# Kernel tuning notes

Hardware: AMD Instinct MI355X
Metric: run time of the kernel (lower is better)

The kernel has to match this reference:

```python
import jax, jax.numpy as jnp
import numpy as np

N = 65536      # total nodes (cells) in batch
E = 262144     # edges per edge type
T = 3          # edge types: row, col, diag
D = 128        # hidden_dim
HG = 4         # gat_heads
DHG = D // HG  # 32, GAT head dim
HH = 4         # hgt_heads
DHH = D // HH  # 32, HGT head dim
B = 32         # boards per batch
SLOPE = 0.2
EPS = 1e-6


def setup_inputs():
    ks = jax.random.split(jax.random.key(0), 32)
    def nrm(i, shape, s=0.05):
        return (jax.random.normal(ks[i], shape) * s).astype(jnp.float32)
    inp = {
        'x_cell': nrm(0, (N, D), 1.0),
        'z_h': nrm(1, (B, D), 1.0),
        'x_cell_embedded': nrm(2, (N, D), 1.0),
        'edge_index': jax.random.randint(ks[3], (T, 2, E), 0, N, dtype=jnp.int32),
        'batch_size': B,
        # GAT conv 1 (one GATConv per edge type, summed)
        'gat1_W': nrm(4, (T, D, D), 0.09),
        'gat1_asrc': nrm(5, (T, HG, DHG), 0.12),
        'gat1_adst': nrm(6, (T, HG, DHG), 0.12),
        'gat1_b': jnp.zeros((T, D), jnp.float32),
        # GAT conv 2
        'gat2_W': nrm(7, (T, D, D), 0.09),
        'gat2_asrc': nrm(8, (T, HG, DHG), 0.12),
        'gat2_adst': nrm(9, (T, HG, DHG), 0.12),
        'gat2_b': jnp.zeros((T, D), jnp.float32),
        # RMSNorms
        'norm1_s': jnp.ones((D,), jnp.float32),
        'norm2_s': jnp.ones((D,), jnp.float32),
        'norm3_s': jnp.ones((D,), jnp.float32),
        # HGT (single node type 'cell', T edge types)
        'hgt_Wk': nrm(10, (D, D), 0.09), 'hgt_bk': jnp.zeros((D,), jnp.float32),
        'hgt_Wq': nrm(11, (D, D), 0.09), 'hgt_bq': jnp.zeros((D,), jnp.float32),
        'hgt_Wv': nrm(12, (D, D), 0.09), 'hgt_bv': jnp.zeros((D,), jnp.float32),
        'hgt_arel': nrm(13, (T, HH, DHH, DHH), 0.15),
        'hgt_mrel': nrm(14, (T, HH, DHH, DHH), 0.15),
        'hgt_prel': jnp.ones((T, HH), jnp.float32),
        'hgt_Wo': nrm(15, (D, D), 0.09), 'hgt_bo': jnp.zeros((D,), jnp.float32),
        'hgt_skip': jnp.ones((), jnp.float32),
        # input injection
        'inj_W': nrm(16, (D, D), 0.09), 'inj_b': jnp.zeros((D,), jnp.float32),
        # FiLM
        'film_W1': nrm(17, (D, 2 * D), 0.09), 'film_b1': jnp.zeros((2 * D,), jnp.float32),
        'film_W2': nrm(18, (2 * D, 2 * D), 0.001), 'film_b2': jnp.zeros((2 * D,), jnp.float32),
    }
    return inp


def _rmsnorm(x, scale):
    return scale * x * jax.lax.rsqrt(jnp.mean(x * x, axis=-1, keepdims=True) + EPS)


def _res(x_old, x_new, scale):
    return jax.nn.leaky_relu(x_old + _rmsnorm(x_new, scale), SLOPE)


def _gat_sum(x, W, asrc, adst, b, src, dst):
    """HeteroConv(sum) over T GATConvs (concat heads, add_self_loops)."""
    loop = jnp.arange(N, dtype=src.dtype)
    def one(Wt, a_s, a_d, bt, s, t):
        s = jnp.concatenate([s, loop])   # self loops
        t = jnp.concatenate([t, loop])
        h = (x @ Wt).reshape(N, HG, DHG)             # [N,H,Dh]
        alpha_src = (h * a_s).sum(-1)                # [N,H]
        alpha_dst = (h * a_d).sum(-1)
        e = jax.nn.leaky_relu(alpha_src[s] + alpha_dst[t], SLOPE)  # [E+N,H]
        m = jax.ops.segment_max(e, t, num_segments=N)
        ex = jnp.exp(e - m[t])
        denom = jax.ops.segment_sum(ex, t, num_segments=N)
        alpha = ex / (denom[t] + 1e-16)
        out = jax.ops.segment_sum(alpha[:, :, None] * h[s], t, num_segments=N)
        return out.reshape(N, D) + bt
    return jax.vmap(one)(W, asrc, adst, b, src, dst).sum(0)


def _hgt(x, Wk, bk, Wq, bq, Wv, bv, a_rel, m_rel, p_rel, Wo, bo, skip, src, dst):
    k = (x @ Wk + bk).reshape(N, HH, DHH)
    q = (x @ Wq + bq).reshape(N, HH, DHH)
    v = (x @ Wv + bv).reshape(N, HH, DHH)
    # per-edge-type relation transforms at node level, then gather per edge
    k_t = jnp.einsum('nhd,thdf->tnhf', k, a_rel)    # [T,N,H,Dk]
    v_t = jnp.einsum('nhd,thdf->tnhf', v, m_rel)
    k_e = jax.vmap(lambda a, i: a[i])(k_t, src)     # [T,E,H,Dk]
    v_e = jax.vmap(lambda a, i: a[i])(v_t, src)
    score = (q[dst] * k_e).sum(-1) * p_rel[:, None, :] / np.sqrt(DHH)  # [T,E,H]
    score = score.reshape(T * E, HH)
    dst_f = dst.reshape(-1)
    m = jax.ops.segment_max(score, dst_f, num_segments=N)
    ex = jnp.exp(score - m[dst_f])
    denom = jax.ops.segment_sum(ex, dst_f, num_segments=N)
    alpha = ex / (denom[dst_f] + 1e-16)
    agg = jax.ops.segment_sum(alpha[:, :, None] * v_e.reshape(T * E, HH, DHH),
                              dst_f, num_segments=N)          # [N,H,Dk]
    out = jax.nn.gelu(agg.reshape(N, D), approximate=False) @ Wo + bo
    sig = jax.nn.sigmoid(skip)
    return sig * out + (1.0 - sig) * x


def _film(nodes, z_h, W1, b1, W2, b2, bsz):
    gb = jax.nn.gelu(z_h @ W1 + b1, approximate=False) @ W2 + b2  # [B,2D]
    gamma, beta = jnp.split(gb, 2, axis=-1)
    gamma = 0.1 * jnp.tanh(gamma)
    beta = 0.1 * jnp.tanh(beta)
    c = N // bsz
    out = (1.0 + gamma)[:, None, :] * nodes.reshape(bsz, c, D) + beta[:, None, :]
    return out.reshape(N, D)


def reference(x_cell, z_h, x_cell_embedded,
              gat1_W, gat1_asrc, gat1_adst, gat1_b,
              gat2_W, gat2_asrc, gat2_adst, gat2_b,
              norm1_s, norm2_s, norm3_s,
              hgt_Wk, hgt_bk, hgt_Wq, hgt_bq, hgt_Wv, hgt_bv,
              hgt_arel, hgt_mrel, hgt_prel, hgt_Wo, hgt_bo, hgt_skip,
              inj_W, inj_b, film_W1, film_b1, film_W2, film_b2,
              edge_index, batch_size):
    src = edge_index[:, 0]
    dst = edge_index[:, 1]
    x1 = _res(x_cell, _gat_sum(x_cell, gat1_W, gat1_asrc, gat1_adst, gat1_b, src, dst), norm1_s)
    x2 = _res(x1, _gat_sum(x1, gat2_W, gat2_asrc, gat2_adst, gat2_b, src, dst), norm2_s)
    x3 = _res(x2, _hgt(x2, hgt_Wk, hgt_bk, hgt_Wq, hgt_bq, hgt_Wv, hgt_bv,
                       hgt_arel, hgt_mrel, hgt_prel, hgt_Wo, hgt_bo, hgt_skip,
                       src, dst), norm3_s)
    x3 = x3 + x_cell_embedded @ inj_W + inj_b
    return _film(x3, z_h, film_W1, film_b1, film_W2, film_b2, batch_size)
```

## Files before the change

### kernel.cpp

```cpp
#include <hip/hip_runtime.h>

#define NN 65536
#define EE 262144
#define ND ((size_t)NN * 128)
#define TBW 132
#define WLP 136

typedef unsigned short u16;
typedef short bf8_t __attribute__((ext_vector_type(8)));
typedef float f32x4 __attribute__((ext_vector_type(4)));

__device__ __forceinline__ float lrelu(float x){ return x > 0.f ? x : 0.2f*x; }
__device__ __forceinline__ float gelu_exact(float x){ return 0.5f*x*(1.f+erff(x*0.70710678118654752f)); }
__device__ __forceinline__ u16 f2bf(float f){
    union { float f; unsigned u; } v; v.f = f;
    unsigned u = v.u;
    return (u16)((u + 0x7FFFu + ((u >> 16) & 1u)) >> 16);
}
__device__ __forceinline__ float bf2f(u16 b){
    union { unsigned u; float f; } v; v.u = ((unsigned)b) << 16; return v.f;
}
__device__ __forceinline__ float2 bf2x(unsigned p){
    union { unsigned u; float f; } a, b;
    a.u = (p & 0xFFFFu) << 16; b.u = p & 0xFFFF0000u;
    return make_float2(a.f, b.f);
}
__device__ __forceinline__ unsigned cvt2(float a, float b){
    unsigned r; asm("v_cvt_pk_bf16_f32 %0, %1, %2" : "=v"(r) : "v"(a), "v"(b)); return r;
}

__device__ __forceinline__ void load_af32(const float* __restrict__ X, int row, int lk, bf8_t* af){
    #pragma unroll
    for (int kk = 0; kk < 4; ++kk){
        const float* p = X + (size_t)row*128 + kk*32 + lk*8;
        float4 a = *(const float4*)p;
        float4 b = *(const float4*)(p+4);
        union { bf8_t v; unsigned u[4]; } r;
        r.u[0] = cvt2(a.x, a.y); r.u[1] = cvt2(a.z, a.w);
        r.u[2] = cvt2(b.x, b.y); r.u[3] = cvt2(b.z, b.w);
        af[kk] = r.v;
    }
}
__device__ __forceinline__ void load_af16(const u16* __restrict__ X, int row, int lk, bf8_t* af){
    #pragma unroll
    for (int kk = 0; kk < 4; ++kk)
        af[kk] = *(const bf8_t*)(X + (size_t)row*128 + kk*32 + lk*8);
}

__device__ __forceinline__ void stage_w(const u16* __restrict__ src, u16* __restrict__ wl, int tid){
    #pragma unroll
    for (int j = 0; j < 8; ++j){
        int o = (j*256 + tid)*8;
        bf8_t v = *(const bf8_t*)(src + o);
        *(bf8_t*)(wl + ((o>>7)*WLP + (o&127))) = v;
    }
}

__device__ __forceinline__ void mfma_l1_acc(const bf8_t* af, const u16* __restrict__ wl,
                                            int lr, int lk, f32x4* acc){
    #pragma unroll
    for (int kk = 0; kk < 4; ++kk){
        bf8_t B[8];
        #pragma unroll
        for (int nt = 0; nt < 8; ++nt)
            B[nt] = *(const bf8_t*)&wl[(nt*16+lr)*WLP + kk*32 + lk*8];
        #pragma unroll
        for (int nt = 0; nt < 8; ++nt)
            acc[nt] = __builtin_amdgcn_mfma_f32_16x16x32_bf16(af[kk], B[nt], acc[nt], 0, 0, 0);
    }
}
__device__ __forceinline__ void mfma_l2_acc(const bf8_t* af0, const bf8_t* af1,
                                            const u16* __restrict__ wl,
                                            int lr, int lk, f32x4* acc0, f32x4* acc1){
    #pragma unroll
    for (int kk = 0; kk < 4; ++kk){
        bf8_t B[8];
        #pragma unroll
        for (int nt = 0; nt < 8; ++nt)
            B[nt] = *(const bf8_t*)&wl[(nt*16+lr)*WLP + kk*32 + lk*8];
        #pragma unroll
        for (int nt = 0; nt < 8; ++nt){
            acc0[nt] = __builtin_amdgcn_mfma_f32_16x16x32_bf16(af0[kk], B[nt], acc0[nt], 0, 0, 0);
            acc1[nt] = __builtin_amdgcn_mfma_f32_16x16x32_bf16(af1[kk], B[nt], acc1[nt], 0, 0, 0);
        }
    }
}
__device__ __forceinline__ void mfma_l2(const bf8_t* af0, const bf8_t* af1,
                                        const u16* __restrict__ wl,
                                        int lr, int lk, f32x4* acc0, f32x4* acc1){
    #pragma unroll
    for (int i = 0; i < 8; ++i){ acc0[i] = (f32x4){0.f,0.f,0.f,0.f}; acc1[i] = (f32x4){0.f,0.f,0.f,0.f}; }
    mfma_l2_acc(af0, af1, wl, lr, lk, acc0, acc1);
}

__device__ __forceinline__ void acc_to_tb(u16 (*tbw)[TBW], const f32x4* acc, int lr, int lk, const float* bias){
    asm volatile("s_waitcnt lgkmcnt(0)" ::: "memory");
    #pragma unroll
    for (int nt = 0; nt < 8; ++nt){
        int col = nt*16 + lr;
        float badd = bias ? bias[col] : 0.f;
        #pragma unroll
        for (int i = 0; i < 4; ++i) tbw[lk*4+i][col] = f2bf(acc[nt][i] + badd);
    }
    asm volatile("s_waitcnt lgkmcnt(0)" ::: "memory");
}
__device__ __forceinline__ void acc_to_tb_gelu(u16 (*tbw)[TBW], const f32x4* acc, int lr, int lk){
    asm volatile("s_waitcnt lgkmcnt(0)" ::: "memory");
    #pragma unroll
    for (int nt = 0; nt < 8; ++nt){
        int col = nt*16 + lr;
        #pragma unroll
        for (int i = 0; i < 4; ++i) tbw[lk*4+i][col] = f2bf(gelu_exact(acc[nt][i]));
    }
    asm volatile("s_waitcnt lgkmcnt(0)" ::: "memory");
}
__device__ __forceinline__ void tb_store(const u16 (*tbw)[TBW], u16* __restrict__ O, size_t rowstride, int rowbase, int lr, int lk){
    #pragma unroll
    for (int c = 0; c < 4; ++c){
        bf8_t v = *(const bf8_t*)&tbw[c*4+lk][lr*8];
        *(bf8_t*)(O + (size_t)(rowbase + c*4 + lk)*rowstride + lr*8) = v;
    }
}
__device__ __forceinline__ void tb_frags(const u16 (*tbw)[TBW], int lr, int lk, bf8_t* ha){
    #pragma unroll
    for (int kk = 0; kk < 4; ++kk) ha[kk] = *(const bf8_t*)&tbw[lr][kk*32 + lk*8];
}
__device__ __forceinline__ void tb_rows(const u16 (*tbw)[TBW], int lr, int lk, bf8_t* rw){
    #pragma unroll
    for (int c = 0; c < 4; ++c) rw[c] = *(const bf8_t*)&tbw[c*4+lk][lr*8];
}

__global__ __launch_bounds__(256) void wpack_k(
    const float* __restrict__ g1W, const float* __restrict__ g2W,
    const float* __restrict__ Wk, const float* __restrict__ Wq, const float* __restrict__ Wv,
    const float* __restrict__ Wo, const float* __restrict__ injW,
    const float* __restrict__ arel, const float* __restrict__ mrel,
    const float* __restrict__ g1as, const float* __restrict__ g1ad,
    const float* __restrict__ g2as, const float* __restrict__ g2ad,
    u16* __restrict__ wp, u16* __restrict__ wpa)
{
    int b = blockIdx.x, tid = threadIdx.x;
    if (b < 17) {
        const float* src; int rel = 0;
        if (b < 3) src = g1W + b*16384;
        else if (b < 6) src = g2W + (b-3)*16384;
        else if (b == 6) src = Wk;
        else if (b == 7) src = Wq;
        else if (b == 8) src = Wv;
        else if (b == 9) src = Wo;
        else if (b == 10) src = injW;
        else if (b < 14) { src = arel + (b-11)*4096; rel = 2; }
        else { src = mrel + (b-14)*4096; rel = 1; }
        u16* dst = wp + (size_t)b*16384;
        for (int idx = tid; idx < 16384; idx += 256) {
            int n = idx >> 7, k = idx & 127;
            float v;
            if (rel == 1)      v = ((n>>5)==(k>>5)) ? src[(n>>5)*1024 + (k&31)*32 + (n&31)] : 0.f;
            else if (rel == 2) v = ((n>>5)==(k>>5)) ? src[(n>>5)*1024 + (n&31)*32 + (k&31)] : 0.f;
            else               v = src[k*128 + n];
            dst[idx] = f2bf(v);
        }
    } else {
        for (int idx = tid; idx < 6*2048; idx += 256) {
            int m = idx >> 11;
            int j = idx & 2047;
            int cg = j >> 7, k = j & 127;
            const float* as = (m < 3) ? g1as : g2as;
            const float* ad = (m < 3) ? g1ad : g2ad;
            int t = (m < 3) ? m : m - 3;
            float v = 0.f;
            if (cg < 4)      { if ((k>>5)==cg)   v = as[t*128 + cg*32 + (k&31)]; }
            else if (cg < 8) { int g = cg-4; if ((k>>5)==g) v = ad[t*128 + g*32 + (k&31)]; }
            wpa[idx] = f2bf(v);
        }
    }
}

template<int AF32>
__global__ __launch_bounds__(256, 2) void gat_gemm3_k(const float* __restrict__ Xf, const u16* __restrict__ Xb,
    const u16* __restrict__ wpg, const u16* __restrict__ wpa,
    u16* __restrict__ hb, float* __restrict__ alsb, float* __restrict__ aldb)
{
    __shared__ __align__(16) u16 wl[128*WLP];
    __shared__ __align__(16) u16 tb[4][16][TBW];
    const int tid = threadIdx.x, wave = tid>>6, lane = tid&63, lr = lane&15, lk = lane>>4;
    const int rw0 = blockIdx.x*128 + wave*32;
    bf8_t af0[4], af1[4];
    if (AF32){ load_af32(Xf, rw0 + lr, lk, af0); load_af32(Xf, rw0 + 16 + lr, lk, af1); }
    else     { load_af16(Xb, rw0 + lr, lk, af0); load_af16(Xb, rw0 + 16 + lr, lk, af1); }
    f32x4 acc0[8], acc1[8];
    for (int t = 0; t < 3; ++t) {
        __syncthreads();
        stage_w(wpg + t*16384, wl, tid);
        __syncthreads();
        mfma_l2(af0, af1, wl, lr, lk, acc0, acc1);
        bf8_t Ba[4];
        #pragma unroll
        for (int kk = 0; kk < 4; ++kk)
            Ba[kk] = *(const bf8_t*)&wpa[t*2048 + lr*128 + kk*32 + lk*8];
        u16* h = hb + (size_t)t*ND;
        float* alst = alsb + (size_t)t*NN*4;
        float* aldt = aldb + (size_t)t*NN*4;
        {
            acc_to_tb(tb[wave], acc0, lr, lk, nullptr);
            tb_store(tb[wave], h, 128, rw0, lr, lk);
            bf8_t ha[4]; tb_frags(tb[wave], lr, lk, ha);
            f32x4 a2 = (f32x4){0.f,0.f,0.f,0.f};
            #pragma unroll
            for (int kk = 0; kk < 4; ++kk)
                a2 = __builtin_amdgcn_mfma_f32_16x16x32_bf16(ha[kk], Ba[kk], a2, 0, 0, 0);
            if (lr < 8){
                float* dp = (lr < 4) ? alst : aldt;
                int g = lr & 3;
                #pragma unroll
                for (int i = 0; i < 4; ++i) dp[(size_t)(rw0 + lk*4 + i)*4 + g] = a2[i];
            }
        }
        {
            acc_to_tb(tb[wave], acc1, lr, lk, nullptr);
            tb_store(tb[wave], h, 128, rw0 + 16, lr, lk);
            bf8_t ha[4]; tb_frags(tb[wave], lr, lk, ha);
            f32x4 a2 = (f32x4){0.f,0.f,0.f,0.f};
            #pragma unroll
            for (int kk = 0; kk < 4; ++kk)
                a2 = __builtin_amdgcn_mfma_f32_16x16x32_bf16(ha[kk], Ba[kk], a2, 0, 0, 0);
            if (lr < 8){
                float* dp = (lr < 4) ? alst : aldt;
                int g = lr & 3;
                #pragma unroll
                for (int i = 0; i < 4; ++i) dp[(size_t)(rw0 + 16 + lk*4 + i)*4 + g] = a2[i];
            }
        }
    }
}

__global__ __launch_bounds__(256, 2) void hgt_proj_k(const u16* __restrict__ X,
    const u16* __restrict__ wpk, const u16* __restrict__ wpq, const u16* __restrict__ wpv,
    const u16* __restrict__ wparel,
    const float* __restrict__ bk, const float* __restrict__ bq, const float* __restrict__ bv,
    u16* __restrict__ kvb, u16* __restrict__ qtb)
{
    __shared__ __align__(16) u16 wl[128*WLP];
    __shared__ __align__(16) u16 tb[4][16][TBW];
    const int tid = threadIdx.x, wave = tid>>6, lane = tid&63, lr = lane&15, lk = lane>>4;
    const int rw0 = blockIdx.x*128 + wave*32;
    bf8_t af0[4], af1[4];
    load_af16(X, rw0 + lr, lk, af0);
    load_af16(X, rw0 + 16 + lr, lk, af1);
    f32x4 acc0[8], acc1[8];
    stage_w(wpk, wl, tid);
    __syncthreads();
    mfma_l2(af0, af1, wl, lr, lk, acc0, acc1);
    acc_to_tb(tb[wave], acc0, lr, lk, bk); tb_store(tb[wave], kvb, 256, rw0, lr, lk);
    acc_to_tb(tb[wave], acc1, lr, lk, bk); tb_store(tb[wave], kvb, 256, rw0 + 16, lr, lk);
    __syncthreads();
    stage_w(wpv, wl, tid);
    __syncthreads();
    mfma_l2(af0, af1, wl, lr, lk, acc0, acc1);
    acc_to_tb(tb[wave], acc0, lr, lk, bv); tb_store(tb[wave], kvb + 128, 256, rw0, lr, lk);
    acc_to_tb(tb[wave], acc1, lr, lk, bv); tb_store(tb[wave], kvb + 128, 256, rw0 + 16, lr, lk);
    __syncthreads();
    stage_w(wpq, wl, tid);
    __syncthreads();
    bf8_t ha0[4], ha1[4];
    mfma_l2(af0, af1, wl, lr, lk, acc0, acc1);
    acc_to_tb(tb[wave], acc0, lr, lk, bq); tb_frags(tb[wave], lr, lk, ha0);
    acc_to_tb(tb[wave], acc1, lr, lk, bq); tb_frags(tb[wave], lr, lk, ha1);
    for (int t = 0; t < 3; ++t){
        __syncthreads();
        stage_w(wparel + t*16384, wl, tid);
        __syncthreads();
        mfma_l2(ha0, ha1, wl, lr, lk, acc0, acc1);
        u16* o = qtb + (size_t)t*ND;
        acc_to_tb(tb[wave], acc0, lr, lk, nullptr); tb_store(tb[wave], o, 128, rw0, lr, lk);
        acc_to_tb(tb[wave], acc1, lr, lk, nullptr); tb_store(tb[wave], o, 128, rw0 + 16, lr, lk);
    }
}

__global__ __launch_bounds__(256) void hgt_agg_k(const u16* __restrict__ kvb,
    const u16* __restrict__ qtb, const float* __restrict__ prel,
    const int* __restrict__ coff, const int* __restrict__ csrc,
    u16* __restrict__ pb)
{
    int gid = blockIdx.x*256 + threadIdx.x;
    int node = gid >> 6, lane = gid & 63;
    int hh = lane >> 4;
    float a0[3], a1[3];
    float dsum = 0.f;
    #pragma unroll
    for (int t = 0; t < 3; ++t) {
        a0[t] = 0.f; a1[t] = 0.f;
        float ph = prel[t*4 + hh] * 0.17677669529663689f;
        float2 qv = bf2x(*(const unsigned*)&qtb[(size_t)t*ND + (size_t)node*128 + lane*2]);
        const int* cs = csrc + (size_t)t*EE;
        int beg = coff[t*(NN+1) + node], end = coff[t*(NN+1) + node + 1];
        int e = beg;
        for (; e + 4 <= end; e += 4) {
            int sA = cs[e], sB = cs[e+1], sC = cs[e+2], sD = cs[e+3];
            size_t rA = (size_t)sA*256 + lane*2, rB = (size_t)sB*256 + lane*2;
            size_t rC = (size_t)sC*256 + lane*2, rD = (size_t)sD*256 + lane*2;
            unsigned kA = *(const unsigned*)&kvb[rA], kB = *(const unsigned*)&kvb[rB];
            unsigned kC = *(const unsigned*)&kvb[rC], kD = *(const unsigned*)&kvb[rD];
            unsigned vA = *(const unsigned*)&kvb[rA+128], vB = *(const unsigned*)&kvb[rB+128];
            unsigned vC = *(const unsigned*)&kvb[rC+128], vD = *(const unsigned*)&kvb[rD+128];
            float2 k2A = bf2x(kA), k2B = bf2x(kB), k2C = bf2x(kC), k2D = bf2x(kD);
            float scA = qv.x*k2A.x + qv.y*k2A.y;
            float scB = qv.x*k2B.x + qv.y*k2B.y;
            float scC = qv.x*k2C.x + qv.y*k2C.y;
            float scD = qv.x*k2D.x + qv.y*k2D.y;
            #pragma unroll
            for (int o = 1; o < 16; o <<= 1){
                scA += __shfl_xor(scA, o); scB += __shfl_xor(scB, o);
                scC += __shfl_xor(scC, o); scD += __shfl_xor(scD, o);
            }
            float eA = expf(scA*ph), eB = expf(scB*ph), eC = expf(scC*ph), eD = expf(scD*ph);
            float2 v2A = bf2x(vA), v2B = bf2x(vB), v2C = bf2x(vC), v2D = bf2x(vD);
            dsum += eA + eB + eC + eD;
            a0[t] += eA*v2A.x + eB*v2B.x + eC*v2C.x + eD*v2D.x;
            a1[t] += eA*v2A.y + eB*v2B.y + eC*v2C.y + eD*v2D.y;
        }
        for (; e < end; ++e) {
            int s = cs[e];
            size_t ro = (size_t)s*256 + lane*2;
            float2 kv = bf2x(*(const unsigned*)&kvb[ro]);
            float sc = qv.x*kv.x + qv.y*kv.y;
            #pragma unroll
            for (int o = 1; o < 16; o <<= 1) sc += __shfl_xor(sc, o);
            float ex = expf(sc * ph);
            float2 vx = bf2x(*(const unsigned*)&kvb[ro + 128]);
            dsum += ex; a0[t] += ex*vx.x; a1[t] += ex*vx.y;
        }
    }
    float inv = 1.f/(dsum + 1e-16f);
    size_t o = (size_t)node*128 + lane*2;
    #pragma unroll
    for (int t = 0; t < 3; ++t)
        *(unsigned*)&pb[(size_t)t*ND + o] = cvt2(a0[t]*inv, a1[t]*inv);
}

__global__ __launch_bounds__(256, 2) void final_k(const u16* __restrict__ pb,
    const u16* __restrict__ wpmrel, const u16* __restrict__ wpo, const float* __restrict__ bo,
    const u16* __restrict__ x2b, const float* __restrict__ skipp, const float* __restrict__ scale,
    const float* __restrict__ xemb, const u16* __restrict__ wpinj, const float* __restrict__ injb,
    const float* __restrict__ gbuf, const int* __restrict__ bszp,
    float* __restrict__ out)
{
    __shared__ __align__(16) u16 wl[128*WLP];
    __shared__ __align__(16) u16 tb[4][16][TBW];
    const int tid = threadIdx.x, wave = tid>>6, lane = tid&63, lr = lane&15, lk = lane>>4;
    const int rw0 = blockIdx.x*128 + wave*32;
    const int rw1 = rw0 + 16;
    f32x4 acc0[8], acc1[8];
    #pragma unroll
    for (int i = 0; i < 8; ++i){ acc0[i] = (f32x4){0.f,0.f,0.f,0.f}; acc1[i] = (f32x4){0.f,0.f,0.f,0.f}; }
    for (int t = 0; t < 3; ++t){
        if (t) __syncthreads();
        stage_w(wpmrel + t*16384, wl, tid);
        __syncthreads();
        bf8_t a0[4], a1[4];
        load_af16(pb + (size_t)t*ND, rw0 + lr, lk, a0);
        load_af16(pb + (size_t)t*ND, rw1 + lr, lk, a1);
        mfma_l2_acc(a0, a1, wl, lr, lk, acc0, acc1);
    }
    bf8_t ga0[4], ga1[4];
    acc_to_tb_gelu(tb[wave], acc0, lr, lk);
    tb_frags(tb[wave], lr, lk, ga0);
    acc_to_tb_gelu(tb[wave], acc1, lr, lk);
    tb_frags(tb[wave], lr, lk, ga1);
    __syncthreads();
    stage_w(wpo, wl, tid);
    __syncthreads();
    mfma_l2(ga0, ga1, wl, lr, lk, acc0, acc1);
    bf8_t hw0[4], hw1[4];
    acc_to_tb(tb[wave], acc0, lr, lk, bo);
    tb_rows(tb[wave], lr, lk, hw0);
    acc_to_tb(tb[wave], acc1, lr, lk, bo);
    tb_rows(tb[wave], lr, lk, hw1);
    bf8_t e0[4], e1[4];
    load_af32(xemb, rw0 + lr, lk, e0);
    load_af32(xemb, rw1 + lr, lk, e1);
    __syncthreads();
    stage_w(wpinj, wl, tid);
    __syncthreads();
    mfma_l2(e0, e1, wl, lr, lk, acc0, acc1);
    bf8_t in0[4], in1[4];
    acc_to_tb(tb[wave], acc0, lr, lk, injb);
    tb_rows(tb[wave], lr, lk, in0);
    acc_to_tb(tb[wave], acc1, lr, lk, injb);
    tb_rows(tb[wave], lr, lk, in1);
    const float sig = 1.f/(1.f + expf(-skipp[0]));
    const int cpb = NN / *bszp;
    float4 sca = *(const float4*)&scale[lr*8];
    float4 scb = *(const float4*)&scale[lr*8 + 4];
    #pragma unroll
    for (int tile = 0; tile < 2; ++tile){
        const bf8_t* hw = tile ? hw1 : hw0;
        const bf8_t* in = tile ? in1 : in0;
        int rwb = tile ? rw1 : rw0;
        #pragma unroll
        for (int c = 0; c < 4; ++c){
            int row = rwb + c*4 + lk;
            bf8_t x8 = *(const bf8_t*)(x2b + (size_t)row*128 + lr*8);
            float x[8], v[8];
            float ssl = 0.f;
            #pragma unroll
            for (int j = 0; j < 8; ++j){
                x[j] = bf2f((u16)x8[j]);
                float h = bf2f((u16)hw[c][j]);
                v[j] = sig*h + (1.f - sig)*x[j];
                ssl += v[j]*v[j];
            }
            ssl += __shfl_xor(ssl, 1); ssl += __shfl_xor(ssl, 2);
            ssl += __shfl_xor(ssl, 4); ssl += __shfl_xor(ssl, 8);
            float rq = rsqrtf(ssl*(1.f/128.f) + 1e-6f);
            const float* gr = gbuf + (row / cpb)*256;
            float4 g0 = *(const float4*)&gr[lr*8];
            float4 g1 = *(const float4*)&gr[lr*8 + 4];
            float4 b0 = *(const float4*)&gr[128 + lr*8];
            float4 b1 = *(const float4*)&gr[128 + lr*8 + 4];
            float4 oA, oB;
            #pragma unroll
            for (int j = 0; j < 8; ++j){
                float scj = (j < 4) ? ((const float*)&sca)[j] : ((const float*)&scb)[j-4];
                float y = lrelu(x[j] + scj*v[j]*rq);
                float hf = y + bf2f((u16)in[c][j]);
                float gj = (j < 4) ? ((const float*)&g0)[j] : ((const float*)&g1)[j-4];
                float bj = (j < 4) ? ((const float*)&b0)[j] : ((const float*)&b1)[j-4];
                float ov = (1.f + gj)*hf + bj;
                if (j < 4) ((float*)&oA)[j] = ov; else ((float*)&oB)[j-4] = ov;
            }
            *(float4*)(out + (size_t)row*128 + lr*8)     = oA;
            *(float4*)(out + (size_t)row*128 + lr*8 + 4) = oB;
        }
    }
}

__global__ __launch_bounds__(256) void hist_k(const int* __restrict__ ei, int* __restrict__ cnt){
    int gid = blockIdx.x*256 + threadIdx.x;
    int t = gid / EE, e = gid - t*EE;
    int d = ei[t*2*EE + EE + e];
    atomicAdd(&cnt[t*NN + d], 1);
}
__global__ __launch_bounds__(256) void scan1_k(const int* __restrict__ cnt, int* __restrict__ off, int* __restrict__ parts){
    __shared__ int sums[256];
    int b = blockIdx.x; int t = b >> 6; int base = (b & 63) * 1024;
    int tid = threadIdx.x;
    int v[4]; int tsum = 0;
    int gbase = t*NN + base + tid*4;
    #pragma unroll
    for (int i = 0; i < 4; ++i){ v[i] = cnt[gbase+i]; tsum += v[i]; }
    sums[tid] = tsum; __syncthreads();
    for (int ofs = 1; ofs < 256; ofs <<= 1) {
        int a = (tid >= ofs) ? sums[tid-ofs] : 0;
        __syncthreads();
        sums[tid] += a;
        __syncthreads();
    }
    int run = sums[tid] - tsum;
    int obase = t*(NN+1) + base + tid*4;
    #pragma unroll
    for (int i = 0; i < 4; ++i){ off[obase+i] = run; run += v[i]; }
    if (tid == 255) parts[b] = sums[255];
}
__global__ void scan2_k(int* parts){
    if (threadIdx.x == 0 && blockIdx.x == 0) {
        for (int t = 0; t < 3; ++t) {
            int run = 0;
            for (int i = 0; i < 64; ++i) { int b = t*64+i; int v = parts[b]; parts[b] = run; run += v; }
        }
    }
}
__global__ __launch_bounds__(256) void scan3_k(int* __restrict__ off, const int* __restrict__ parts){
    int b = blockIdx.x; int t = b >> 6; int base = (b & 63) * 1024;
    int add = parts[b];
    int idx = t*(NN+1) + base + threadIdx.x*4;
    #pragma unroll
    for (int i = 0; i < 4; ++i) off[idx+i] += add;
    if (threadIdx.x == 0 && (b & 63) == 0) off[t*(NN+1) + NN] = EE;
}
__global__ __launch_bounds__(256) void scatter_k(const int* __restrict__ ei, const int* __restrict__ off,
                                                 int* __restrict__ cur, int* __restrict__ out){
    int gid = blockIdx.x*256 + threadIdx.x;
    int t = gid / EE, e = gid - t*EE;
    int s = ei[t*2*EE + e];
    int d = ei[t*2*EE + EE + e];
    int p = atomicAdd(&cur[t*NN + d], 1);
    out[t*EE + off[t*(NN+1)+d] + p] = s;
}

template<int XF32>
__global__ __launch_bounds__(256) void gat_aggres_k(const u16* __restrict__ hb,
    const float* __restrict__ alsb, const float* __restrict__ aldb,
    const int* __restrict__ coff, const int* __restrict__ csrc,
    const float* __restrict__ bias3, const float* __restrict__ xoldf, const u16* __restrict__ xoldb,
    const float* __restrict__ scale, u16* __restrict__ outb)
{
    int gid = blockIdx.x*256 + threadIdx.x;
    int node = gid >> 6, lane = gid & 63;
    int g = lane >> 4;
    float a0 = 0.f, a1 = 0.f;
    for (int t = 0; t < 3; ++t) {
        const u16* h = hb + (size_t)t*ND;
        const float* als = alsb + (size_t)t*NN*4;
        float ad = aldb[(size_t)t*NN*4 + node*4 + g];
        float aself = als[node*4 + g];
        const int* cs = csrc + (size_t)t*EE;
        int beg = coff[t*(NN+1) + node], end = coff[t*(NN+1) + node + 1];
        float ex = expf(lrelu(aself + ad));
        float dsum = ex;
        float2 hv = bf2x(*(const unsigned*)&h[(size_t)node*128 + lane*2]);
        float s0 = ex*hv.x, s1 = ex*hv.y;
        int e = beg;
        for (; e + 4 <= end; e += 4) {
            int sA = cs[e], sB = cs[e+1], sC = cs[e+2], sD = cs[e+3];
            unsigned hA = *(const unsigned*)&h[(size_t)sA*128 + lane*2];
            unsigned hB = *(const unsigned*)&h[(size_t)sB*128 + lane*2];
            unsigned hC = *(const unsigned*)&h[(size_t)sC*128 + lane*2];
            unsigned hD = *(const unsigned*)&h[(size_t)sD*128 + lane*2];
            float aA = als[sA*4+g], aB = als[sB*4+g], aC = als[sC*4+g], aD = als[sD*4+g];
            float eA = expf(lrelu(aA + ad)), eB = expf(lrelu(aB + ad));
            float eC = expf(lrelu(aC + ad)), eD = expf(lrelu(aD + ad));
            float2 wA = bf2x(hA), wB = bf2x(hB), wC = bf2x(hC), wD = bf2x(hD);
            dsum += eA + eB + eC + eD;
            s0 += eA*wA.x + eB*wB.x + eC*wC.x + eD*wD.x;
            s1 += eA*wA.y + eB*wB.y + eC*wC.y + eD*wD.y;
        }
        for (; e < end; ++e) {
            int s = cs[e];
            unsigned hp = *(const unsigned*)&h[(size_t)s*128 + lane*2];
            float av = als[s*4 + g];
            float exx = expf(lrelu(av + ad));
            float2 hw = bf2x(hp);
            dsum += exx; s0 += exx*hw.x; s1 += exx*hw.y;
        }
        float inv = 1.f/(dsum + 1e-16f);
        a0 += s0*inv; a1 += s1*inv;
    }
    int c0 = lane*2;
    a0 += bias3[c0]   + bias3[128+c0]   + bias3[256+c0];
    a1 += bias3[c0+1] + bias3[128+c0+1] + bias3[256+c0+1];
    float ssum = a0*a0 + a1*a1;
    #pragma unroll
    for (int o = 1; o < 64; o <<= 1) ssum += __shfl_xor(ssum, o);
    float r = rsqrtf(ssum*(1.f/128.f) + 1e-6f);
    size_t off = (size_t)node*128 + c0;
    float2 xo;
    if (XF32) xo = *(const float2*)&xoldf[off];
    else      xo = bf2x(*(const unsigned*)&xoldb[off]);
    float y0 = lrelu(xo.x + scale[c0]*a0*r);
    float y1 = lrelu(xo.y + scale[c0+1]*a1*r);
    *(unsigned*)&outb[off] = cvt2(y0, y1);
}

__global__ __launch_bounds__(256) void film_k(const float* __restrict__ z,
    const float* __restrict__ W1, const float* __restrict__ b1,
    const float* __restrict__ W2, const float* __restrict__ b2,
    float* __restrict__ gb)
{
    __shared__ float zr[128];
    __shared__ float g1[256];
    int r = blockIdx.x, tid = threadIdx.x;
    if (tid < 128) zr[tid] = z[r*128 + tid];
    __syncthreads();
    float s = b1[tid];
    for (int k = 0; k < 128; ++k) s += zr[k]*W1[k*256 + tid];
    g1[tid] = gelu_exact(s);
    __syncthreads();
    float s2 = b2[tid];
    for (int k = 0; k < 256; ++k) s2 += g1[k]*W2[k*256 + tid];
    gb[r*256 + tid] = 0.1f*tanhf(s2);
}

extern "C" void kernel_launch(void* const* d_in, const int* in_sizes, int n_in,
                              void* d_out, int out_size, void* d_ws, size_t ws_size,
                              hipStream_t stream)
{
    const float* x_cell = (const float*)d_in[0];
    const float* z_h    = (const float*)d_in[1];
    const float* x_emb  = (const float*)d_in[2];
    const int*   eidx   = (const int*)d_in[3];
    const int*   bszp   = (const int*)d_in[4];
    const float* g1W  = (const float*)d_in[5];
    const float* g1as = (const float*)d_in[6];
    const float* g1ad = (const float*)d_in[7];
    const float* g1b  = (const float*)d_in[8];
    const float* g2W  = (const float*)d_in[9];
    const float* g2as = (const float*)d_in[10];
    const float* g2ad = (const float*)d_in[11];
    const float* g2b  = (const float*)d_in[12];
    const float* n1s  = (const float*)d_in[13];
    const float* n2s  = (const float*)d_in[14];
    const float* n3s  = (const float*)d_in[15];
    const float* Wk   = (const float*)d_in[16];
    const float* bk   = (const float*)d_in[17];
    const float* Wq   = (const float*)d_in[18];
    const float* bq   = (const float*)d_in[19];
    const float* Wv   = (const float*)d_in[20];
    const float* bv   = (const float*)d_in[21];
    const float* arel = (const float*)d_in[22];
    const float* mrel = (const float*)d_in[23];
    const float* prel = (const float*)d_in[24];
    const float* Wo   = (const float*)d_in[25];
    const float* bo   = (const float*)d_in[26];
    const float* skipp= (const float*)d_in[27];
    const float* injW = (const float*)d_in[28];
    const float* injb = (const float*)d_in[29];
    const float* fW1  = (const float*)d_in[30];
    const float* fb1  = (const float*)d_in[31];
    const float* fW2  = (const float*)d_in[32];
    const float* fb2  = (const float*)d_in[33];

    u16* wp   = (u16*)d_ws;
    u16* wpa  = wp + (size_t)17*16384;
    u16* x1b  = wpa + 6*2048;
    u16* x2b  = x1b + ND;
    u16* kvb  = x2b + ND;
    u16* pb   = kvb + 2*ND;
    u16* hb   = pb + 3*ND;
    float* alsb = (float*)(hb + 3*ND);
    float* aldb = alsb + (size_t)3*NN*4;
    float* gbuf = aldb + (size_t)3*NN*4;
    int* coff   = (int*)(gbuf + 32*256);
    int* csrc   = coff + 3*(NN+1);
    int* tmpc   = csrc + 3*EE;
    int* parts  = tmpc + 3*NN;

    u16* qtb = hb;
    float* outp = (float*)d_out;

    const u16* wpg1 = wp;
    const u16* wpg2 = wp + (size_t)3*16384;
    const u16* wpk  = wp + (size_t)6*16384;
    const u16* wpq  = wp + (size_t)7*16384;
    const u16* wpv  = wp + (size_t)8*16384;
    const u16* wpo  = wp + (size_t)9*16384;
    const u16* wpinj= wp + (size_t)10*16384;
    const u16* wparel = wp + (size_t)11*16384;
    const u16* wpmrel = wp + (size_t)14*16384;

    wpack_k<<<18, 256, 0, stream>>>(g1W, g2W, Wk, Wq, Wv, Wo, injW, arel, mrel,
                                    g1as, g1ad, g2as, g2ad, wp, wpa);

    hipMemsetAsync(tmpc, 0, 3*NN*sizeof(int), stream);
    hist_k<<<3*EE/256, 256, 0, stream>>>(eidx, tmpc);
    scan1_k<<<192, 256, 0, stream>>>(tmpc, coff, parts);
    scan2_k<<<1, 64, 0, stream>>>(parts);
    scan3_k<<<192, 256, 0, stream>>>(coff, parts);
    hipMemsetAsync(tmpc, 0, 3*NN*sizeof(int), stream);
    scatter_k<<<3*EE/256, 256, 0, stream>>>(eidx, coff, tmpc, csrc);

    int B = in_sizes[1] / 128;
    film_k<<<B, 256, 0, stream>>>(z_h, fW1, fb1, fW2, fb2, gbuf);

    gat_gemm3_k<1><<<512, 256, 0, stream>>>(x_cell, nullptr, wpg1, wpa, hb, alsb, aldb);
    gat_aggres_k<1><<<16384, 256, 0, stream>>>(hb, alsb, aldb, coff, csrc, g1b, x_cell, nullptr, n1s, x1b);

    gat_gemm3_k<0><<<512, 256, 0, stream>>>(nullptr, x1b, wpg2, wpa + 3*2048, hb, alsb, aldb);
    gat_aggres_k<0><<<16384, 256, 0, stream>>>(hb, alsb, aldb, coff, csrc, g2b, nullptr, x1b, n2s, x2b);

    hgt_proj_k<<<512, 256, 0, stream>>>(x2b, wpk, wpq, wpv, wparel,
                                        bk, bq, bv, kvb, qtb);
    hgt_agg_k<<<16384, 256, 0, stream>>>(kvb, qtb, prel, coff, csrc, pb);

    final_k<<<512, 256, 0, stream>>>(pb, wpmrel, wpo, bo, x2b, skipp, n3s,
                                     x_emb, wpinj, injb, gbuf, bszp, outp);
}
```

Before: 572.5 us.

## Merge per-type CSR into one tagged CSR and split GEMM kernels across grid

```diff
diff --git a/kernel.cpp b/kernel.cpp
--- a/kernel.cpp
+++ b/kernel.cpp
@@ -69,9 +69,17 @@
             acc[nt] = __builtin_amdgcn_mfma_f32_16x16x32_bf16(af[kk], B[nt], acc[nt], 0, 0, 0);
     }
 }
-__device__ __forceinline__ void mfma_l2_acc(const bf8_t* af0, const bf8_t* af1,
-                                            const u16* __restrict__ wl,
-                                            int lr, int lk, f32x4* acc0, f32x4* acc1){
+__device__ __forceinline__ void mfma_l1(const bf8_t* af, const u16* __restrict__ wl,
+                                        int lr, int lk, f32x4* acc){
+    #pragma unroll
+    for (int i = 0; i < 8; ++i) acc[i] = (f32x4){0.f,0.f,0.f,0.f};
+    mfma_l1_acc(af, wl, lr, lk, acc);
+}
+__device__ __forceinline__ void mfma_l2(const bf8_t* af0, const bf8_t* af1,
+                                        const u16* __restrict__ wl,
+                                        int lr, int lk, f32x4* acc0, f32x4* acc1){
+    #pragma unroll
+    for (int i = 0; i < 8; ++i){ acc0[i] = (f32x4){0.f,0.f,0.f,0.f}; acc1[i] = (f32x4){0.f,0.f,0.f,0.f}; }
     #pragma unroll
     for (int kk = 0; kk < 4; ++kk){
         bf8_t B[8];
@@ -84,13 +92,6 @@
             acc1[nt] = __builtin_amdgcn_mfma_f32_16x16x32_bf16(af1[kk], B[nt], acc1[nt], 0, 0, 0);
         }
     }
-}
-__device__ __forceinline__ void mfma_l2(const bf8_t* af0, const bf8_t* af1,
-                                        const u16* __restrict__ wl,
-                                        int lr, int lk, f32x4* acc0, f32x4* acc1){
-    #pragma unroll
-    for (int i = 0; i < 8; ++i){ acc0[i] = (f32x4){0.f,0.f,0.f,0.f}; acc1[i] = (f32x4){0.f,0.f,0.f,0.f}; }
-    mfma_l2_acc(af0, af1, wl, lr, lk, acc0, acc1);
 }
 
 __device__ __forceinline__ void acc_to_tb(u16 (*tbw)[TBW], const f32x4* acc, int lr, int lk, const float* bias){
@@ -177,64 +178,62 @@
 }
 
 template<int AF32>
-__global__ __launch_bounds__(256, 2) void gat_gemm3_k(const float* __restrict__ Xf, const u16* __restrict__ Xb,
+__global__ __launch_bounds__(256, 3) void gat_gemm3_k(const float* __restrict__ Xf, const u16* __restrict__ Xb,
     const u16* __restrict__ wpg, const u16* __restrict__ wpa,
     u16* __restrict__ hb, float* __restrict__ alsb, float* __restrict__ aldb)
 {
     __shared__ __align__(16) u16 wl[128*WLP];
     __shared__ __align__(16) u16 tb[4][16][TBW];
     const int tid = threadIdx.x, wave = tid>>6, lane = tid&63, lr = lane&15, lk = lane>>4;
+    const int t = blockIdx.y;
     const int rw0 = blockIdx.x*128 + wave*32;
     bf8_t af0[4], af1[4];
     if (AF32){ load_af32(Xf, rw0 + lr, lk, af0); load_af32(Xf, rw0 + 16 + lr, lk, af1); }
     else     { load_af16(Xb, rw0 + lr, lk, af0); load_af16(Xb, rw0 + 16 + lr, lk, af1); }
+    stage_w(wpg + t*16384, wl, tid);
+    bf8_t Ba[4];
+    #pragma unroll
+    for (int kk = 0; kk < 4; ++kk)
+        Ba[kk] = *(const bf8_t*)&wpa[t*2048 + lr*128 + kk*32 + lk*8];
+    __syncthreads();
     f32x4 acc0[8], acc1[8];
-    for (int t = 0; t < 3; ++t) {
-        __syncthreads();
-        stage_w(wpg + t*16384, wl, tid);
-        __syncthreads();
-        mfma_l2(af0, af1, wl, lr, lk, acc0, acc1);
-        bf8_t Ba[4];
+    mfma_l2(af0, af1, wl, lr, lk, acc0, acc1);
+    u16* h = hb + (size_t)t*ND;
+    float* alst = alsb + (size_t)t*NN*4;
+    float* aldt = aldb + (size_t)t*NN*4;
+    {
+        acc_to_tb(tb[wave], acc0, lr, lk, nullptr);
+        tb_store(tb[wave], h, 128, rw0, lr, lk);
+        bf8_t ha[4]; tb_frags(tb[wave], lr, lk, ha);
+        f32x4 a2 = (f32x4){0.f,0.f,0.f,0.f};
         #pragma unroll
         for (int kk = 0; kk < 4; ++kk)
-            Ba[kk] = *(const bf8_t*)&wpa[t*2048 + lr*128 + kk*32 + lk*8];
-        u16* h = hb + (size_t)t*ND;
-        float* alst = alsb + (size_t)t*NN*4;
-        float* aldt = aldb + (size_t)t*NN*4;
-        {
-            acc_to_tb(tb[wave], acc0, lr, lk, nullptr);
-            tb_store(tb[wave], h, 128, rw0, lr, lk);
-            bf8_t ha[4]; tb_frags(tb[wave], lr, lk, ha);
-            f32x4 a2 = (f32x4){0.f,0.f,0.f,0.f};
+            a2 = __builtin_amdgcn_mfma_f32_16x16x32_bf16(ha[kk], Ba[kk], a2, 0, 0, 0);
+        if (lr < 8){
+            float* dp = (lr < 4) ? alst : aldt;
+            int g = lr & 3;
             #pragma unroll
-            for (int kk = 0; kk < 4; ++kk)
-                a2 = __builtin_amdgcn_mfma_f32_16x16x32_bf16(ha[kk], Ba[kk], a2, 0, 0, 0);
-            if (lr < 8){
-                float* dp = (lr < 4) ? alst : aldt;
-                int g = lr & 3;
-                #pragma unroll
-                for (int i = 0; i < 4; ++i) dp[(size_t)(rw0 + lk*4 + i)*4 + g] = a2[i];
-            }
-        }
-        {
-            acc_to_tb(tb[wave], acc1, lr, lk, nullptr);
-            tb_store(tb[wave], h, 128, rw0 + 16, lr, lk);
-            bf8_t ha[4]; tb_frags(tb[wave], lr, lk, ha);
-            f32x4 a2 = (f32x4){0.f,0.f,0.f,0.f};
+            for (int i = 0; i < 4; ++i) dp[(size_t)(rw0 + lk*4 + i)*4 + g] = a2[i];
+        }
+    }
+    {
+        acc_to_tb(tb[wave], acc1, lr, lk, nullptr);
+        tb_store(tb[wave], h, 128, rw0 + 16, lr, lk);
+        bf8_t ha[4]; tb_frags(tb[wave], lr, lk, ha);
+        f32x4 a2 = (f32x4){0.f,0.f,0.f,0.f};
+        #pragma unroll
+        for (int kk = 0; kk < 4; ++kk)
+            a2 = __builtin_amdgcn_mfma_f32_16x16x32_bf16(ha[kk], Ba[kk], a2, 0, 0, 0);
+        if (lr < 8){
+            float* dp = (lr < 4) ? alst : aldt;
+            int g = lr & 3;
             #pragma unroll
-            for (int kk = 0; kk < 4; ++kk)
-                a2 = __builtin_amdgcn_mfma_f32_16x16x32_bf16(ha[kk], Ba[kk], a2, 0, 0, 0);
-            if (lr < 8){
-                float* dp = (lr < 4) ? alst : aldt;
-                int g = lr & 3;
-                #pragma unroll
-                for (int i = 0; i < 4; ++i) dp[(size_t)(rw0 + 16 + lk*4 + i)*4 + g] = a2[i];
-            }
-        }
-    }
-}
-
-__global__ __launch_bounds__(256, 2) void hgt_proj_k(const u16* __restrict__ X,
+            for (int i = 0; i < 4; ++i) dp[(size_t)(rw0 + 16 + lk*4 + i)*4 + g] = a2[i];
+        }
+    }
+}
+
+__global__ __launch_bounds__(256, 3) void hgt_proj_k(const u16* __restrict__ X,
     const u16* __restrict__ wpk, const u16* __restrict__ wpq, const u16* __restrict__ wpv,
     const u16* __restrict__ wparel,
     const float* __restrict__ bk, const float* __restrict__ bq, const float* __restrict__ bv,
@@ -243,30 +242,32 @@
     __shared__ __align__(16) u16 wl[128*WLP];
     __shared__ __align__(16) u16 tb[4][16][TBW];
     const int tid = threadIdx.x, wave = tid>>6, lane = tid&63, lr = lane&15, lk = lane>>4;
+    const int task = blockIdx.y;
     const int rw0 = blockIdx.x*128 + wave*32;
     bf8_t af0[4], af1[4];
     load_af16(X, rw0 + lr, lk, af0);
     load_af16(X, rw0 + 16 + lr, lk, af1);
     f32x4 acc0[8], acc1[8];
-    stage_w(wpk, wl, tid);
-    __syncthreads();
-    mfma_l2(af0, af1, wl, lr, lk, acc0, acc1);
-    acc_to_tb(tb[wave], acc0, lr, lk, bk); tb_store(tb[wave], kvb, 256, rw0, lr, lk);
-    acc_to_tb(tb[wave], acc1, lr, lk, bk); tb_store(tb[wave], kvb, 256, rw0 + 16, lr, lk);
-    __syncthreads();
-    stage_w(wpv, wl, tid);
-    __syncthreads();
-    mfma_l2(af0, af1, wl, lr, lk, acc0, acc1);
-    acc_to_tb(tb[wave], acc0, lr, lk, bv); tb_store(tb[wave], kvb + 128, 256, rw0, lr, lk);
-    acc_to_tb(tb[wave], acc1, lr, lk, bv); tb_store(tb[wave], kvb + 128, 256, rw0 + 16, lr, lk);
-    __syncthreads();
-    stage_w(wpq, wl, tid);
-    __syncthreads();
-    bf8_t ha0[4], ha1[4];
-    mfma_l2(af0, af1, wl, lr, lk, acc0, acc1);
-    acc_to_tb(tb[wave], acc0, lr, lk, bq); tb_frags(tb[wave], lr, lk, ha0);
-    acc_to_tb(tb[wave], acc1, lr, lk, bq); tb_frags(tb[wave], lr, lk, ha1);
-    for (int t = 0; t < 3; ++t){
+    if (task == 0) {
+        stage_w(wpk, wl, tid);
+        __syncthreads();
+        mfma_l2(af0, af1, wl, lr, lk, acc0, acc1);
+        acc_to_tb(tb[wave], acc0, lr, lk, bk); tb_store(tb[wave], kvb, 256, rw0, lr, lk);
+        acc_to_tb(tb[wave], acc1, lr, lk, bk); tb_store(tb[wave], kvb, 256, rw0 + 16, lr, lk);
+    } else if (task == 1) {
+        stage_w(wpv, wl, tid);
+        __syncthreads();
+        mfma_l2(af0, af1, wl, lr, lk, acc0, acc1);
+        acc_to_tb(tb[wave], acc0, lr, lk, bv); tb_store(tb[wave], kvb + 128, 256, rw0, lr, lk);
+        acc_to_tb(tb[wave], acc1, lr, lk, bv); tb_store(tb[wave], kvb + 128, 256, rw0 + 16, lr, lk);
+    } else {
+        const int t = task - 2;
+        stage_w(wpq, wl, tid);
+        __syncthreads();
+        mfma_l2(af0, af1, wl, lr, lk, acc0, acc1);
+        bf8_t ha0[4], ha1[4];
+        acc_to_tb(tb[wave], acc0, lr, lk, bq); tb_frags(tb[wave], lr, lk, ha0);
+        acc_to_tb(tb[wave], acc1, lr, lk, bq); tb_frags(tb[wave], lr, lk, ha1);
         __syncthreads();
         stage_w(wparel + t*16384, wl, tid);
         __syncthreads();
@@ -279,66 +280,77 @@
 
 __global__ __launch_bounds__(256) void hgt_agg_k(const u16* __restrict__ kvb,
     const u16* __restrict__ qtb, const float* __restrict__ prel,
-    const int* __restrict__ coff, const int* __restrict__ csrc,
+    const int* __restrict__ moff, const int* __restrict__ msrc,
     u16* __restrict__ pb)
 {
     int gid = blockIdx.x*256 + threadIdx.x;
     int node = gid >> 6, lane = gid & 63;
     int hh = lane >> 4;
-    float a0[3], a1[3];
+    const float S = 0.17677669529663689f;
+    float2 qv0 = bf2x(*(const unsigned*)&qtb[(size_t)node*128 + lane*2]);
+    float2 qv1 = bf2x(*(const unsigned*)&qtb[ND + (size_t)node*128 + lane*2]);
+    float2 qv2 = bf2x(*(const unsigned*)&qtb[2*ND + (size_t)node*128 + lane*2]);
+    float ph0 = prel[hh]*S, ph1 = prel[4+hh]*S, ph2 = prel[8+hh]*S;
     float dsum = 0.f;
-    #pragma unroll
-    for (int t = 0; t < 3; ++t) {
-        a0[t] = 0.f; a1[t] = 0.f;
-        float ph = prel[t*4 + hh] * 0.17677669529663689f;
-        float2 qv = bf2x(*(const unsigned*)&qtb[(size_t)t*ND + (size_t)node*128 + lane*2]);
-        const int* cs = csrc + (size_t)t*EE;
-        int beg = coff[t*(NN+1) + node], end = coff[t*(NN+1) + node + 1];
-        int e = beg;
-        for (; e + 4 <= end; e += 4) {
-            int sA = cs[e], sB = cs[e+1], sC = cs[e+2], sD = cs[e+3];
-            size_t rA = (size_t)sA*256 + lane*2, rB = (size_t)sB*256 + lane*2;
-            size_t rC = (size_t)sC*256 + lane*2, rD = (size_t)sD*256 + lane*2;
-            unsigned kA = *(const unsigned*)&kvb[rA], kB = *(const unsigned*)&kvb[rB];
-            unsigned kC = *(const unsigned*)&kvb[rC], kD = *(const unsigned*)&kvb[rD];
-            unsigned vA = *(const unsigned*)&kvb[rA+128], vB = *(const unsigned*)&kvb[rB+128];
-            unsigned vC = *(const unsigned*)&kvb[rC+128], vD = *(const unsigned*)&kvb[rD+128];
-            float2 k2A = bf2x(kA), k2B = bf2x(kB), k2C = bf2x(kC), k2D = bf2x(kD);
-            float scA = qv.x*k2A.x + qv.y*k2A.y;
-            float scB = qv.x*k2B.x + qv.y*k2B.y;
-            float scC = qv.x*k2C.x + qv.y*k2C.y;
-            float scD = qv.x*k2D.x + qv.y*k2D.y;
-            #pragma unroll
-            for (int o = 1; o < 16; o <<= 1){
-                scA += __shfl_xor(scA, o); scB += __shfl_xor(scB, o);
-                scC += __shfl_xor(scC, o); scD += __shfl_xor(scD, o);
-            }
-            float eA = expf(scA*ph), eB = expf(scB*ph), eC = expf(scC*ph), eD = expf(scD*ph);
-            float2 v2A = bf2x(vA), v2B = bf2x(vB), v2C = bf2x(vC), v2D = bf2x(vD);
-            dsum += eA + eB + eC + eD;
-            a0[t] += eA*v2A.x + eB*v2B.x + eC*v2C.x + eD*v2D.x;
-            a1[t] += eA*v2A.y + eB*v2B.y + eC*v2C.y + eD*v2D.y;
-        }
-        for (; e < end; ++e) {
-            int s = cs[e];
-            size_t ro = (size_t)s*256 + lane*2;
-            float2 kv = bf2x(*(const unsigned*)&kvb[ro]);
-            float sc = qv.x*kv.x + qv.y*kv.y;
+    float a00=0.f,a01=0.f,a10=0.f,a11=0.f,a20=0.f,a21=0.f;
+    int beg = moff[node], end = moff[node+1];
+    int e = beg;
+    for (; e + 8 <= end; e += 8) {
+        int sp[8]; unsigned kw[8], vw[8];
+        #pragma unroll
+        for (int j = 0; j < 8; ++j) sp[j] = msrc[e+j];
+        #pragma unroll
+        for (int j = 0; j < 8; ++j){
+            size_t ro = (size_t)(sp[j] & 0xFFFF)*256 + lane*2;
+            kw[j] = *(const unsigned*)&kvb[ro];
+            vw[j] = *(const unsigned*)&kvb[ro + 128];
+        }
+        #pragma unroll
+        for (int j = 0; j < 8; ++j){
+            int tt = sp[j] >> 16;
+            float qx = tt==0 ? qv0.x : (tt==1 ? qv1.x : qv2.x);
+            float qy = tt==0 ? qv0.y : (tt==1 ? qv1.y : qv2.y);
+            float2 k2 = bf2x(kw[j]);
+            float sc = qx*k2.x + qy*k2.y;
             #pragma unroll
             for (int o = 1; o < 16; o <<= 1) sc += __shfl_xor(sc, o);
+            float ph = tt==0 ? ph0 : (tt==1 ? ph1 : ph2);
             float ex = expf(sc * ph);
-            float2 vx = bf2x(*(const unsigned*)&kvb[ro + 128]);
-            dsum += ex; a0[t] += ex*vx.x; a1[t] += ex*vx.y;
-        }
+            float2 v2 = bf2x(vw[j]);
+            float e0 = tt==0?ex:0.f, e1 = tt==1?ex:0.f, e2 = tt==2?ex:0.f;
+            dsum += ex;
+            a00 += e0*v2.x; a01 += e0*v2.y;
+            a10 += e1*v2.x; a11 += e1*v2.y;
+            a20 += e2*v2.x; a21 += e2*v2.y;
+        }
+    }
+    for (; e < end; ++e) {
+        int sp = msrc[e];
+        int tt = sp >> 16;
+        size_t ro = (size_t)(sp & 0xFFFF)*256 + lane*2;
+        float2 k2 = bf2x(*(const unsigned*)&kvb[ro]);
+        float qx = tt==0 ? qv0.x : (tt==1 ? qv1.x : qv2.x);
+        float qy = tt==0 ? qv0.y : (tt==1 ? qv1.y : qv2.y);
+        float sc = qx*k2.x + qy*k2.y;
+        #pragma unroll
+        for (int o = 1; o < 16; o <<= 1) sc += __shfl_xor(sc, o);
+        float ph = tt==0 ? ph0 : (tt==1 ? ph1 : ph2);
+        float ex = expf(sc * ph);
+        float2 v2 = bf2x(*(const unsigned*)&kvb[ro + 128]);
+        float e0 = tt==0?ex:0.f, e1 = tt==1?ex:0.f, e2 = tt==2?ex:0.f;
+        dsum += ex;
+        a00 += e0*v2.x; a01 += e0*v2.y;
+        a10 += e1*v2.x; a11 += e1*v2.y;
+        a20 += e2*v2.x; a21 += e2*v2.y;
     }
     float inv = 1.f/(dsum + 1e-16f);
     size_t o = (size_t)node*128 + lane*2;
-    #pragma unroll
-    for (int t = 0; t < 3; ++t)
-        *(unsigned*)&pb[(size_t)t*ND + o] = cvt2(a0[t]*inv, a1[t]*inv);
-}
-
-__global__ __launch_bounds__(256, 2) void final_k(const u16* __restrict__ pb,
+    *(unsigned*)&pb[o]        = cvt2(a00*inv, a01*inv);
+    *(unsigned*)&pb[ND + o]   = cvt2(a10*inv, a11*inv);
+    *(unsigned*)&pb[2*ND + o] = cvt2(a20*inv, a21*inv);
+}
+
+__global__ __launch_bounds__(256, 3) void final_k(const u16* __restrict__ pb,
     const u16* __restrict__ wpmrel, const u16* __restrict__ wpo, const float* __restrict__ bo,
     const u16* __restrict__ x2b, const float* __restrict__ skipp, const float* __restrict__ scale,
     const float* __restrict__ xemb, const u16* __restrict__ wpinj, const float* __restrict__ injb,
@@ -348,90 +360,74 @@
     __shared__ __align__(16) u16 wl[128*WLP];
     __shared__ __align__(16) u16 tb[4][16][TBW];
     const int tid = threadIdx.x, wave = tid>>6, lane = tid&63, lr = lane&15, lk = lane>>4;
-    const int rw0 = blockIdx.x*128 + wave*32;
-    const int rw1 = rw0 + 16;
-    f32x4 acc0[8], acc1[8];
-    #pragma unroll
-    for (int i = 0; i < 8; ++i){ acc0[i] = (f32x4){0.f,0.f,0.f,0.f}; acc1[i] = (f32x4){0.f,0.f,0.f,0.f}; }
+    const int rw = blockIdx.x*64 + wave*16;
+    f32x4 acc[8];
+    #pragma unroll
+    for (int i = 0; i < 8; ++i) acc[i] = (f32x4){0.f,0.f,0.f,0.f};
     for (int t = 0; t < 3; ++t){
         if (t) __syncthreads();
+        bf8_t a0[4]; load_af16(pb + (size_t)t*ND, rw + lr, lk, a0);
         stage_w(wpmrel + t*16384, wl, tid);
         __syncthreads();
-        bf8_t a0[4], a1[4];
-        load_af16(pb + (size_t)t*ND, rw0 + lr, lk, a0);
-        load_af16(pb + (size_t)t*ND, rw1 + lr, lk, a1);
-        mfma_l2_acc(a0, a1, wl, lr, lk, acc0, acc1);
-    }
-    bf8_t ga0[4], ga1[4];
-    acc_to_tb_gelu(tb[wave], acc0, lr, lk);
-    tb_frags(tb[wave], lr, lk, ga0);
-    acc_to_tb_gelu(tb[wave], acc1, lr, lk);
-    tb_frags(tb[wave], lr, lk, ga1);
+        mfma_l1_acc(a0, wl, lr, lk, acc);
+    }
+    bf8_t ga[4];
+    acc_to_tb_gelu(tb[wave], acc, lr, lk);
+    tb_frags(tb[wave], lr, lk, ga);
     __syncthreads();
     stage_w(wpo, wl, tid);
     __syncthreads();
-    mfma_l2(ga0, ga1, wl, lr, lk, acc0, acc1);
-    bf8_t hw0[4], hw1[4];
-    acc_to_tb(tb[wave], acc0, lr, lk, bo);
-    tb_rows(tb[wave], lr, lk, hw0);
-    acc_to_tb(tb[wave], acc1, lr, lk, bo);
-    tb_rows(tb[wave], lr, lk, hw1);
-    bf8_t e0[4], e1[4];
-    load_af32(xemb, rw0 + lr, lk, e0);
-    load_af32(xemb, rw1 + lr, lk, e1);
+    mfma_l1(ga, wl, lr, lk, acc);
+    bf8_t hw[4];
+    acc_to_tb(tb[wave], acc, lr, lk, bo);
+    tb_rows(tb[wave], lr, lk, hw);
+    bf8_t e0[4];
+    load_af32(xemb, rw + lr, lk, e0);
     __syncthreads();
     stage_w(wpinj, wl, tid);
     __syncthreads();
-    mfma_l2(e0, e1, wl, lr, lk, acc0, acc1);
-    bf8_t in0[4], in1[4];
-    acc_to_tb(tb[wave], acc0, lr, lk, injb);
-    tb_rows(tb[wave], lr, lk, in0);
-    acc_to_tb(tb[wave], acc1, lr, lk, injb);
-    tb_rows(tb[wave], lr, lk, in1);
+    mfma_l1(e0, wl, lr, lk, acc);
+    bf8_t in[4];
+    acc_to_tb(tb[wave], acc, lr, lk, injb);
+    tb_rows(tb[wave], lr, lk, in);
     const float sig = 1.f/(1.f + expf(-skipp[0]));
     const int cpb = NN / *bszp;
     float4 sca = *(const float4*)&scale[lr*8];
     float4 scb = *(const float4*)&scale[lr*8 + 4];
     #pragma unroll
-    for (int tile = 0; tile < 2; ++tile){
-        const bf8_t* hw = tile ? hw1 : hw0;
-        const bf8_t* in = tile ? in1 : in0;
-        int rwb = tile ? rw1 : rw0;
-        #pragma unroll
-        for (int c = 0; c < 4; ++c){
-            int row = rwb + c*4 + lk;
-            bf8_t x8 = *(const bf8_t*)(x2b + (size_t)row*128 + lr*8);
-            float x[8], v[8];
-            float ssl = 0.f;
-            #pragma unroll
-            for (int j = 0; j < 8; ++j){
-                x[j] = bf2f((u16)x8[j]);
-                float h = bf2f((u16)hw[c][j]);
-                v[j] = sig*h + (1.f - sig)*x[j];
-                ssl += v[j]*v[j];
-            }
-            ssl += __shfl_xor(ssl, 1); ssl += __shfl_xor(ssl, 2);
-            ssl += __shfl_xor(ssl, 4); ssl += __shfl_xor(ssl, 8);
-            float rq = rsqrtf(ssl*(1.f/128.f) + 1e-6f);
-            const float* gr = gbuf + (row / cpb)*256;
-            float4 g0 = *(const float4*)&gr[lr*8];
-            float4 g1 = *(const float4*)&gr[lr*8 + 4];
-            float4 b0 = *(const float4*)&gr[128 + lr*8];
-            float4 b1 = *(const float4*)&gr[128 + lr*8 + 4];
-            float4 oA, oB;
-            #pragma unroll
-            for (int j = 0; j < 8; ++j){
-                float scj = (j < 4) ? ((const float*)&sca)[j] : ((const float*)&scb)[j-4];
-                float y = lrelu(x[j] + scj*v[j]*rq);
-                float hf = y + bf2f((u16)in[c][j]);
-                float gj = (j < 4) ? ((const float*)&g0)[j] : ((const float*)&g1)[j-4];
-                float bj = (j < 4) ? ((const float*)&b0)[j] : ((const float*)&b1)[j-4];
-                float ov = (1.f + gj)*hf + bj;
-                if (j < 4) ((float*)&oA)[j] = ov; else ((float*)&oB)[j-4] = ov;
-            }
-            *(float4*)(out + (size_t)row*128 + lr*8)     = oA;
-            *(float4*)(out + (size_t)row*128 + lr*8 + 4) = oB;
-        }
+    for (int c = 0; c < 4; ++c){
+        int row = rw + c*4 + lk;
+        bf8_t x8 = *(const bf8_t*)(x2b + (size_t)row*128 + lr*8);
+        float x[8], v[8];
+        float ssl = 0.f;
+        #pragma unroll
+        for (int j = 0; j < 8; ++j){
+            x[j] = bf2f((u16)x8[j]);
+            float h = bf2f((u16)hw[c][j]);
+            v[j] = sig*h + (1.f - sig)*x[j];
+            ssl += v[j]*v[j];
+        }
+        ssl += __shfl_xor(ssl, 1); ssl += __shfl_xor(ssl, 2);
+        ssl += __shfl_xor(ssl, 4); ssl += __shfl_xor(ssl, 8);
+        float rq = rsqrtf(ssl*(1.f/128.f) + 1e-6f);
+        const float* gr = gbuf + (row / cpb)*256;
+        float4 g0 = *(const float4*)&gr[lr*8];
+        float4 g1 = *(const float4*)&gr[lr*8 + 4];
+        float4 b0 = *(const float4*)&gr[128 + lr*8];
+        float4 b1 = *(const float4*)&gr[128 + lr*8 + 4];
+        float4 oA, oB;
+        #pragma unroll
+        for (int j = 0; j < 8; ++j){
+            float scj = (j < 4) ? ((const float*)&sca)[j] : ((const float*)&scb)[j-4];
+            float y = lrelu(x[j] + scj*v[j]*rq);
+            float hf = y + bf2f((u16)in[c][j]);
+            float gj = (j < 4) ? ((const float*)&g0)[j] : ((const float*)&g1)[j-4];
+            float bj = (j < 4) ? ((const float*)&b0)[j] : ((const float*)&b1)[j-4];
+            float ov = (1.f + gj)*hf + bj;
+            if (j < 4) ((float*)&oA)[j] = ov; else ((float*)&oB)[j-4] = ov;
+        }
+        *(float4*)(out + (size_t)row*128 + lr*8)     = oA;
+        *(float4*)(out + (size_t)row*128 + lr*8 + 4) = oB;
     }
 }
 
@@ -439,14 +435,14 @@
     int gid = blockIdx.x*256 + threadIdx.x;
     int t = gid / EE, e = gid - t*EE;
     int d = ei[t*2*EE + EE + e];
-    atomicAdd(&cnt[t*NN + d], 1);
+    atomicAdd(&cnt[d], 1);
 }
 __global__ __launch_bounds__(256) void scan1_k(const int* __restrict__ cnt, int* __restrict__ off, int* __restrict__ parts){
     __shared__ int sums[256];
-    int b = blockIdx.x; int t = b >> 6; int base = (b & 63) * 1024;
+    int b = blockIdx.x; int base = b * 1024;
     int tid = threadIdx.x;
     int v[4]; int tsum = 0;
-    int gbase = t*NN + base + tid*4;
+    int gbase = base + tid*4;
     #pragma unroll
     for (int i = 0; i < 4; ++i){ v[i] = cnt[gbase+i]; tsum += v[i]; }
     sums[tid] = tsum; __syncthreads();
@@ -457,26 +453,24 @@
         __syncthreads();
     }
     int run = sums[tid] - tsum;
-    int obase = t*(NN+1) + base + tid*4;
+    int obase = base + tid*4;
     #pragma unroll
     for (int i = 0; i < 4; ++i){ off[obase+i] = run; run += v[i]; }
     if (tid == 255) parts[b] = sums[255];
 }
 __global__ void scan2_k(int* parts){
     if (threadIdx.x == 0 && blockIdx.x == 0) {
-        for (int t = 0; t < 3; ++t) {
-            int run = 0;
-            for (int i = 0; i < 64; ++i) { int b = t*64+i; int v = parts[b]; parts[b] = run; run += v; }
-        }
+        int run = 0;
+        for (int i = 0; i < 64; ++i) { int v = parts[i]; parts[i] = run; run += v; }
     }
 }
 __global__ __launch_bounds__(256) void scan3_k(int* __restrict__ off, const int* __restrict__ parts){
-    int b = blockIdx.x; int t = b >> 6; int base = (b & 63) * 1024;
+    int b = blockIdx.x; int base = b * 1024;
     int add = parts[b];
-    int idx = t*(NN+1) + base + threadIdx.x*4;
+    int idx = base + threadIdx.x*4;
     #pragma unroll
     for (int i = 0; i < 4; ++i) off[idx+i] += add;
-    if (threadIdx.x == 0 && (b & 63) == 0) off[t*(NN+1) + NN] = EE;
+    if (b == 0 && threadIdx.x == 0) off[NN] = 3*EE;
 }
 __global__ __launch_bounds__(256) void scatter_k(const int* __restrict__ ei, const int* __restrict__ off,
                                                  int* __restrict__ cur, int* __restrict__ out){
@@ -484,58 +478,79 @@
     int t = gid / EE, e = gid - t*EE;
     int s = ei[t*2*EE + e];
     int d = ei[t*2*EE + EE + e];
-    int p = atomicAdd(&cur[t*NN + d], 1);
-    out[t*EE + off[t*(NN+1)+d] + p] = s;
+    int p = atomicAdd(&cur[d], 1);
+    out[off[d] + p] = s | (t << 16);
 }
 
 template<int XF32>
 __global__ __launch_bounds__(256) void gat_aggres_k(const u16* __restrict__ hb,
     const float* __restrict__ alsb, const float* __restrict__ aldb,
-    const int* __restrict__ coff, const int* __restrict__ csrc,
+    const int* __restrict__ moff, const int* __restrict__ msrc,
     const float* __restrict__ bias3, const float* __restrict__ xoldf, const u16* __restrict__ xoldb,
     const float* __restrict__ scale, u16* __restrict__ outb)
 {
     int gid = blockIdx.x*256 + threadIdx.x;
     int node = gid >> 6, lane = gid & 63;
     int g = lane >> 4;
-    float a0 = 0.f, a1 = 0.f;
-    for (int t = 0; t < 3; ++t) {
-        const u16* h = hb + (size_t)t*ND;
-        const float* als = alsb + (size_t)t*NN*4;
-        float ad = aldb[(size_t)t*NN*4 + node*4 + g];
-        float aself = als[node*4 + g];
-        const int* cs = csrc + (size_t)t*EE;
-        int beg = coff[t*(NN+1) + node], end = coff[t*(NN+1) + node + 1];
-        float ex = expf(lrelu(aself + ad));
-        float dsum = ex;
-        float2 hv = bf2x(*(const unsigned*)&h[(size_t)node*128 + lane*2]);
-        float s0 = ex*hv.x, s1 = ex*hv.y;
-        int e = beg;
-        for (; e + 4 <= end; e += 4) {
-            int sA = cs[e], sB = cs[e+1], sC = cs[e+2], sD = cs[e+3];
-            unsigned hA = *(const unsigned*)&h[(size_t)sA*128 + lane*2];
-            unsigned hB = *(const unsigned*)&h[(size_t)sB*128 + lane*2];
-            unsigned hC = *(const unsigned*)&h[(size_t)sC*128 + lane*2];
-            unsigned hD = *(const unsigned*)&h[(size_t)sD*128 + lane*2];
-            float aA = als[sA*4+g], aB = als[sB*4+g], aC = als[sC*4+g], aD = als[sD*4+g];
-            float eA = expf(lrelu(aA + ad)), eB = expf(lrelu(aB + ad));
-            float eC = expf(lrelu(aC + ad)), eD = expf(lrelu(aD + ad));
-            float2 wA = bf2x(hA), wB = bf2x(hB), wC = bf2x(hC), wD = bf2x(hD);
-            dsum += eA + eB + eC + eD;
-            s0 += eA*wA.x + eB*wB.x + eC*wC.x + eD*wD.x;
-            s1 += eA*wA.y + eB*wB.y + eC*wC.y + eD*wD.y;
-        }
-        for (; e < end; ++e) {
-            int s = cs[e];
-            unsigned hp = *(const unsigned*)&h[(size_t)s*128 + lane*2];
-            float av = als[s*4 + g];
-            float exx = expf(lrelu(av + ad));
-            float2 hw = bf2x(hp);
-            dsum += exx; s0 += exx*hw.x; s1 += exx*hw.y;
-        }
-        float inv = 1.f/(dsum + 1e-16f);
-        a0 += s0*inv; a1 += s1*inv;
-    }
+    float ad0 = aldb[(size_t)node*4 + g];
+    float ad1 = aldb[((size_t)NN + node)*4 + g];
+    float ad2 = aldb[((size_t)2*NN + node)*4 + g];
+    float dsum0, dsum1, dsum2, s00, s01, s10, s11, s20, s21;
+    {
+        float ex = expf(lrelu(alsb[(size_t)node*4 + g] + ad0));
+        float2 hv = bf2x(*(const unsigned*)&hb[(size_t)node*128 + lane*2]);
+        dsum0 = ex; s00 = ex*hv.x; s01 = ex*hv.y;
+    }
+    {
+        float ex = expf(lrelu(alsb[((size_t)NN + node)*4 + g] + ad1));
+        float2 hv = bf2x(*(const unsigned*)&hb[((size_t)NN + node)*128 + lane*2]);
+        dsum1 = ex; s10 = ex*hv.x; s11 = ex*hv.y;
+    }
+    {
+        float ex = expf(lrelu(alsb[((size_t)2*NN + node)*4 + g] + ad2));
+        float2 hv = bf2x(*(const unsigned*)&hb[((size_t)2*NN + node)*128 + lane*2]);
+        dsum2 = ex; s20 = ex*hv.x; s21 = ex*hv.y;
+    }
+    int beg = moff[node], end = moff[node+1];
+    int e = beg;
+    for (; e + 8 <= end; e += 8) {
+        int sp[8]; unsigned hp[8]; float av[8];
+        #pragma unroll
+        for (int j = 0; j < 8; ++j) sp[j] = msrc[e+j];
+        #pragma unroll
+        for (int j = 0; j < 8; ++j){
+            hp[j] = *(const unsigned*)&hb[(size_t)sp[j]*128 + lane*2];
+            av[j] = alsb[(size_t)sp[j]*4 + g];
+        }
+        #pragma unroll
+        for (int j = 0; j < 8; ++j){
+            int tt = sp[j] >> 16;
+            float adt = tt==0 ? ad0 : (tt==1 ? ad1 : ad2);
+            float ex = expf(lrelu(av[j] + adt));
+            float2 w = bf2x(hp[j]);
+            float e0 = tt==0?ex:0.f, e1 = tt==1?ex:0.f, e2 = tt==2?ex:0.f;
+            dsum0 += e0; dsum1 += e1; dsum2 += e2;
+            s00 += e0*w.x; s01 += e0*w.y;
+            s10 += e1*w.x; s11 += e1*w.y;
+            s20 += e2*w.x; s21 += e2*w.y;
+        }
+    }
+    for (; e < end; ++e) {
+        int sp = msrc[e];
+        int tt = sp >> 16;
+        unsigned hp = *(const unsigned*)&hb[(size_t)sp*128 + lane*2];
+        float av = alsb[(size_t)sp*4 + g];
+        float adt = tt==0 ? ad0 : (tt==1 ? ad1 : ad2);
+        float ex = expf(lrelu(av + adt));
+        float2 w = bf2x(hp);
+        float e0 = tt==0?ex:0.f, e1 = tt==1?ex:0.f, e2 = tt==2?ex:0.f;
+        dsum0 += e0; dsum1 += e1; dsum2 += e2;
+        s00 += e0*w.x; s01 += e0*w.y;
+        s10 += e1*w.x; s11 += e1*w.y;
+        s20 += e2*w.x; s21 += e2*w.y;
+    }
+    float a0 = s00/(dsum0+1e-16f) + s10/(dsum1+1e-16f) + s20/(dsum2+1e-16f);
+    float a1 = s01/(dsum0+1e-16f) + s11/(dsum1+1e-16f) + s21/(dsum2+1e-16f);
     int c0 = lane*2;
     a0 += bias3[c0]   + bias3[128+c0]   + bias3[256+c0];
     a1 += bias3[c0+1] + bias3[128+c0+1] + bias3[256+c0+1];
@@ -641,27 +656,27 @@
     wpack_k<<<18, 256, 0, stream>>>(g1W, g2W, Wk, Wq, Wv, Wo, injW, arel, mrel,
                                     g1as, g1ad, g2as, g2ad, wp, wpa);
 
-    hipMemsetAsync(tmpc, 0, 3*NN*sizeof(int), stream);
+    hipMemsetAsync(tmpc, 0, NN*sizeof(int), stream);
     hist_k<<<3*EE/256, 256, 0, stream>>>(eidx, tmpc);
-    scan1_k<<<192, 256, 0, stream>>>(tmpc, coff, parts);
+    scan1_k<<<64, 256, 0, stream>>>(tmpc, coff, parts);
     scan2_k<<<1, 64, 0, stream>>>(parts);
-    scan3_k<<<192, 256, 0, stream>>>(coff, parts);
-    hipMemsetAsync(tmpc, 0, 3*NN*sizeof(int), stream);
+    scan3_k<<<64, 256, 0, stream>>>(coff, parts);
+    hipMemsetAsync(tmpc, 0, NN*sizeof(int), stream);
     scatter_k<<<3*EE/256, 256, 0, stream>>>(eidx, coff, tmpc, csrc);
 
     int B = in_sizes[1] / 128;
     film_k<<<B, 256, 0, stream>>>(z_h, fW1, fb1, fW2, fb2, gbuf);
 
-    gat_gemm3_k<1><<<512, 256, 0, stream>>>(x_cell, nullptr, wpg1, wpa, hb, alsb, aldb);
+    gat_gemm3_k<1><<<dim3(512,3), 256, 0, stream>>>(x_cell, nullptr, wpg1, wpa, hb, alsb, aldb);
     gat_aggres_k<1><<<16384, 256, 0, stream>>>(hb, alsb, aldb, coff, csrc, g1b, x_cell, nullptr, n1s, x1b);
 
-    gat_gemm3_k<0><<<512, 256, 0, stream>>>(nullptr, x1b, wpg2, wpa + 3*2048, hb, alsb, aldb);
+    gat_gemm3_k<0><<<dim3(512,3), 256, 0, stream>>>(nullptr, x1b, wpg2, wpa + 3*2048, hb, alsb, aldb);
     gat_aggres_k<0><<<16384, 256, 0, stream>>>(hb, alsb, aldb, coff, csrc, g2b, nullptr, x1b, n2s, x2b);
 
-    hgt_proj_k<<<512, 256, 0, stream>>>(x2b, wpk, wpq, wpv, wparel,
-                                        bk, bq, bv, kvb, qtb);
+    hgt_proj_k<<<dim3(512,5), 256, 0, stream>>>(x2b, wpk, wpq, wpv, wparel,
+                                                bk, bq, bv, kvb, qtb);
     hgt_agg_k<<<16384, 256, 0, stream>>>(kvb, qtb, prel, coff, csrc, pb);
 
-    final_k<<<512, 256, 0, stream>>>(pb, wpmrel, wpo, bo, x2b, skipp, n3s,
-                                     x_emb, wpinj, injb, gbuf, bszp, outp);
-}
+    final_k<<<1024, 256, 0, stream>>>(pb, wpmrel, wpo, bo, x2b, skipp, n3s,
+                                      x_emb, wpinj, injb, gbuf, bszp, outp);
+}
```

Measured after the change: 620.6 us. +8.4%, slower.
